# Performance work log

Measured on AMD Instinct MI355X. Metric: run time of the kernel, lower is better.

Reference implementation:

```python
import jax, jax.numpy as jnp
import numpy as np

N = 100000      # num nodes
E = 1600000     # num edges
F_IN = 602      # Reddit input features
H = 256         # num_hidden
C = 42          # num_classes


def gcn_conv(x, src, dst, W, b, num_nodes):
    """PyG GCNConv: add self loops, symmetric deg^-1/2 normalization, scatter-add."""
    h = x @ W  # [N, out] dense transform first (PyG order)
    self_idx = jnp.arange(num_nodes, dtype=src.dtype)
    s = jnp.concatenate([src, self_idx])  # [E+N]
    d = jnp.concatenate([dst, self_idx])
    deg = jax.ops.segment_sum(jnp.ones_like(d, dtype=h.dtype), d, num_segments=num_nodes)
    dinv = deg ** -0.5  # deg >= 1 due to self loops
    norm = dinv[s] * dinv[d]  # [E+N]
    msg = h[s] * norm[:, None]  # [E+N, out] gather + scale
    out = jax.ops.segment_sum(msg, d, num_segments=num_nodes)  # scatter-add
    return out + b


def setup_inputs() -> dict:
    key = jax.random.key(0)
    k = jax.random.split(key, 5)
    x = jax.random.normal(k[0], (N, F_IN), dtype=jnp.float32)
    edge_index = jax.random.randint(k[1], (2, E), 0, N, dtype=jnp.int32)
    # Glorot-style init for GCNConv linear weights; bias zeros (PyG default)
    W1 = jax.random.normal(k[2], (F_IN, H), dtype=jnp.float32) * np.float32(1.0 / np.sqrt(F_IN))
    b1 = jnp.zeros((H,), dtype=jnp.float32)
    W2 = jax.random.normal(k[3], (H, C), dtype=jnp.float32) * np.float32(1.0 / np.sqrt(H))
    b2 = jnp.zeros((C,), dtype=jnp.float32)
    return {"x": x, "edge_index": edge_index, "W1": W1, "b1": b1, "W2": W2, "b2": b2}


def reference(x, edge_index, W1, b1, W2, b2):
    src, dst = edge_index[0], edge_index[1]
    num_nodes = x.shape[0]
    h = gcn_conv(x, src, dst, W1, b1, num_nodes)
    h = jax.nn.relu(h)
    # dropout is identity in eval mode (deterministic reference)
    out = gcn_conv(h, src, dst, W2, b2, num_nodes)
    return jax.nn.log_softmax(out, axis=1)
```

## Files before the change

kernel.cpp:

```cpp
#include <hip/hip_runtime.h>
#include <stdint.h>

#define NN 100000
#define NE 1600000
#define FIN 602
#define KP1 608
#define H 256
#define C 42
#define NP2 48
#define NB1 98

typedef __bf16 bf16;
typedef __bf16 bf16x8 __attribute__((ext_vector_type(8)));
typedef float f32x4 __attribute__((ext_vector_type(4)));

__device__ __forceinline__ float b2f(bf16 v) { return (float)v; }
__device__ __forceinline__ bf16 f2b(float v) { return (bf16)v; }
__device__ __forceinline__ float us2f(unsigned short u) {
    union { unsigned int i; float f; } w; w.i = ((unsigned int)u) << 16; return w.f;
}


__global__ void k_zero(int* __restrict__ p, int n) {
    int i = blockIdx.x * 256 + threadIdx.x;
    if (i < n) p[i] = 0;
}

__global__ void k_count(const int* __restrict__ dst, int* __restrict__ cnt) {
    int e = blockIdx.x * 256 + threadIdx.x;
    if (e < NE) atomicAdd(&cnt[dst[e]], 1);
}

__global__ void k_dinv(const int* __restrict__ cnt, float* __restrict__ dinv) {
    int i = blockIdx.x * 256 + threadIdx.x;
    if (i < NN) dinv[i] = rsqrtf((float)(cnt[i] + 1));
}

__global__ __launch_bounds__(256) void k_scan1(const int* __restrict__ cnt,
                                               int* __restrict__ excl, int* __restrict__ bsum) {
    __shared__ int ts[256];
    const int tid = threadIdx.x;
    const int base = blockIdx.x * 1024 + tid * 4;
    int v[4];
#pragma unroll
    for (int j = 0; j < 4; ++j) v[j] = (base + j < NN) ? cnt[base + j] : 0;
    int s = v[0] + v[1] + v[2] + v[3];
    ts[tid] = s;
    __syncthreads();
    for (int off = 1; off < 256; off <<= 1) {
        int t = (tid >= off) ? ts[tid - off] : 0;
        __syncthreads();
        if (tid >= off) ts[tid] += t;
        __syncthreads();
    }
    int prefix = ts[tid] - s;
    if (tid == 255) bsum[blockIdx.x] = ts[255];
    int run = prefix;
#pragma unroll
    for (int j = 0; j < 4; ++j) {
        if (base + j < NN) excl[base + j] = run;
        run += v[j];
    }
}

__global__ __launch_bounds__(128) void k_scan2(int* __restrict__ bsum) {
    __shared__ int ts[128];
    const int tid = threadIdx.x;
    int v = (tid < NB1) ? bsum[tid] : 0;
    ts[tid] = v;
    __syncthreads();
    for (int off = 1; off < 128; off <<= 1) {
        int t = (tid >= off) ? ts[tid - off] : 0;
        __syncthreads();
        if (tid >= off) ts[tid] += t;
        __syncthreads();
    }
    if (tid < NB1) bsum[tid] = ts[tid] - v;
}

__global__ __launch_bounds__(256) void k_scan3(const int* __restrict__ excl, const int* __restrict__ bsum,
                                               int* __restrict__ rowptr, int* __restrict__ cursor) {
    const int tid = threadIdx.x;
    const int base = blockIdx.x * 1024 + tid * 4;
    const int add = bsum[blockIdx.x];
#pragma unroll
    for (int j = 0; j < 4; ++j) {
        int i = base + j;
        if (i < NN) { int r = excl[i] + add; rowptr[i] = r; cursor[i] = r; }
    }
    if (blockIdx.x == 0 && tid == 0) rowptr[NN] = NE;
}

__global__ void k_fill(const int* __restrict__ src, const int* __restrict__ dst,
                       int* __restrict__ cursor, int* __restrict__ esrc) {
    int e = blockIdx.x * 256 + threadIdx.x;
    if (e < NE) {
        int d = dst[e];
        int pos = atomicAdd(&cursor[d], 1);
        esrc[pos] = src[e];
    }
}


__global__ void k_transpose_w1(const float* __restrict__ w1, bf16* __restrict__ w1t) {
    int idx = blockIdx.x * 256 + threadIdx.x;
    int n = idx / KP1;
    int k = idx % KP1;
    w1t[idx] = (k < FIN) ? f2b(w1[(size_t)k * H + n]) : (bf16)0.0f;
}

__global__ void k_transpose_w2(const float* __restrict__ w2, bf16* __restrict__ w2t) {
    int idx = blockIdx.x * 256 + threadIdx.x;
    int n = idx >> 8;
    int k = idx & 255;
    w2t[idx] = (n < C) ? f2b(w2[(size_t)k * C + n]) : (bf16)0.0f;
}


__global__ __launch_bounds__(256) void k_gemm1(const float* __restrict__ x,
                                               const bf16* __restrict__ w1t,
                                               bf16* __restrict__ h1) {
    __shared__ bf16 As[64 * 32];
    const int tid = threadIdx.x;
    const int wave = tid >> 6;
    const int lane = tid & 63;
    const int q = lane >> 4;
    const int r = lane & 15;
    const int row0 = blockIdx.x * 64;

    const int srow = tid >> 2;
    const int sseg = tid & 3;
    int gsrow = row0 + srow;
    if (gsrow >= NN) gsrow = NN - 1;
    const float* xrow = x + (size_t)gsrow * FIN + sseg * 8;

    f32x4 acc[4][4];
#pragma unroll
    for (int a = 0; a < 4; ++a)
#pragma unroll
        for (int b = 0; b < 4; ++b) acc[a][b] = (f32x4){0.f, 0.f, 0.f, 0.f};

    const bf16* bbase = w1t + (size_t)(wave * 64) * KP1;

    for (int kk = 0; kk < 19; ++kk) {
        const int k0 = kk * 32;
        const int c0 = k0 + sseg * 8;
        union { bf16 s[8]; uint4 u; } pk;
        if (c0 + 8 <= FIN) {
            const float2* p = (const float2*)(xrow + k0);
            float2 f0 = p[0], f1 = p[1], f2 = p[2], f3 = p[3];
            pk.s[0] = f2b(f0.x); pk.s[1] = f2b(f0.y);
            pk.s[2] = f2b(f1.x); pk.s[3] = f2b(f1.y);
            pk.s[4] = f2b(f2.x); pk.s[5] = f2b(f2.y);
            pk.s[6] = f2b(f3.x); pk.s[7] = f2b(f3.y);
        } else {
#pragma unroll
            for (int j = 0; j < 8; ++j)
                pk.s[j] = (c0 + j < FIN) ? f2b(xrow[k0 + j]) : (bf16)0.0f;
        }
        __syncthreads();
        *(uint4*)(As + srow * 32 + sseg * 8) = pk.u;
        __syncthreads();

        bf16x8 af[4];
#pragma unroll
        for (int rt = 0; rt < 4; ++rt) {
            union { uint4 u; bf16x8 v; } ua;
            ua.u = *(const uint4*)(As + (rt * 16 + r) * 32 + q * 8);
            af[rt] = ua.v;
        }
#pragma unroll
        for (int ct = 0; ct < 4; ++ct) {
            const bf16* bp = bbase + (size_t)(ct * 16 + r) * KP1 + k0 + q * 8;
            union { uint4 u; bf16x8 v; } ub;
            ub.u = *(const uint4*)bp;
#pragma unroll
            for (int rt = 0; rt < 4; ++rt)
                acc[rt][ct] = __builtin_amdgcn_mfma_f32_16x16x32_bf16(af[rt], ub.v, acc[rt][ct], 0, 0, 0);
        }
    }

#pragma unroll
    for (int rt = 0; rt < 4; ++rt) {
#pragma unroll
        for (int ct = 0; ct < 4; ++ct) {
            const int col = wave * 64 + ct * 16 + r;
#pragma unroll
            for (int rr = 0; rr < 4; ++rr) {
                const int m = row0 + rt * 16 + q * 4 + rr;
                if (m < NN) h1[(size_t)m * H + col] = f2b(acc[rt][ct][rr]);
            }
        }
    }
}


__global__ __launch_bounds__(64) void k_gather1(const int* __restrict__ rowptr,
                                                const int* __restrict__ esrc,
                                                const bf16* __restrict__ h1,
                                                const float* __restrict__ dinv,
                                                const float* __restrict__ b1,
                                                bf16* __restrict__ hb) {
    const int n = blockIdx.x;
    const int tid = threadIdx.x;
    const float dn = dinv[n];

    uint2 u = ((const uint2*)(h1 + (size_t)n * H))[tid];
    float ws = dn * dn;
    float a0 = us2f((unsigned short)(u.x & 0xffff)) * ws;
    float a1 = us2f((unsigned short)(u.x >> 16)) * ws;
    float a2 = us2f((unsigned short)(u.y & 0xffff)) * ws;
    float a3 = us2f((unsigned short)(u.y >> 16)) * ws;

    const int beg = rowptr[n], end = rowptr[n + 1];
    int j = beg;
    for (; j + 3 < end; j += 4) {
        int s0 = esrc[j], s1 = esrc[j + 1], s2 = esrc[j + 2], s3 = esrc[j + 3];
        float w0 = dinv[s0] * dn, w1 = dinv[s1] * dn, w2 = dinv[s2] * dn, w3 = dinv[s3] * dn;
        uint2 v0 = ((const uint2*)(h1 + (size_t)s0 * H))[tid];
        uint2 v1 = ((const uint2*)(h1 + (size_t)s1 * H))[tid];
        uint2 v2 = ((const uint2*)(h1 + (size_t)s2 * H))[tid];
        uint2 v3 = ((const uint2*)(h1 + (size_t)s3 * H))[tid];
        a0 += us2f((unsigned short)(v0.x & 0xffff)) * w0;
        a1 += us2f((unsigned short)(v0.x >> 16)) * w0;
        a2 += us2f((unsigned short)(v0.y & 0xffff)) * w0;
        a3 += us2f((unsigned short)(v0.y >> 16)) * w0;
        a0 += us2f((unsigned short)(v1.x & 0xffff)) * w1;
        a1 += us2f((unsigned short)(v1.x >> 16)) * w1;
        a2 += us2f((unsigned short)(v1.y & 0xffff)) * w1;
        a3 += us2f((unsigned short)(v1.y >> 16)) * w1;
        a0 += us2f((unsigned short)(v2.x & 0xffff)) * w2;
        a1 += us2f((unsigned short)(v2.x >> 16)) * w2;
        a2 += us2f((unsigned short)(v2.y & 0xffff)) * w2;
        a3 += us2f((unsigned short)(v2.y >> 16)) * w2;
        a0 += us2f((unsigned short)(v3.x & 0xffff)) * w3;
        a1 += us2f((unsigned short)(v3.x >> 16)) * w3;
        a2 += us2f((unsigned short)(v3.y & 0xffff)) * w3;
        a3 += us2f((unsigned short)(v3.y >> 16)) * w3;
    }
    for (; j < end; ++j) {
        int s = esrc[j];
        float w = dinv[s] * dn;
        uint2 v = ((const uint2*)(h1 + (size_t)s * H))[tid];
        a0 += us2f((unsigned short)(v.x & 0xffff)) * w;
        a1 += us2f((unsigned short)(v.x >> 16)) * w;
        a2 += us2f((unsigned short)(v.y & 0xffff)) * w;
        a3 += us2f((unsigned short)(v.y >> 16)) * w;
    }

    float4 bb = ((const float4*)b1)[tid];
    a0 += bb.x; a1 += bb.y; a2 += bb.z; a3 += bb.w;
    a0 = a0 > 0.f ? a0 : 0.f;
    a1 = a1 > 0.f ? a1 : 0.f;
    a2 = a2 > 0.f ? a2 : 0.f;
    a3 = a3 > 0.f ? a3 : 0.f;

    union { unsigned short s[4]; uint2 u; } pk;
    union { bf16 b; unsigned short s; } cv;
    cv.b = f2b(a0); pk.s[0] = cv.s;
    cv.b = f2b(a1); pk.s[1] = cv.s;
    cv.b = f2b(a2); pk.s[2] = cv.s;
    cv.b = f2b(a3); pk.s[3] = cv.s;
    ((uint2*)(hb + (size_t)n * H))[tid] = pk.u;
}


__global__ __launch_bounds__(256) void k_gemm2(const bf16* __restrict__ hb,
                                               const bf16* __restrict__ w2t,
                                               bf16* __restrict__ h2) {
    __shared__ bf16 As[256 * 32];
    const int tid = threadIdx.x;
    const int wave = tid >> 6;
    const int lane = tid & 63;
    const int q = lane >> 4;
    const int r = lane & 15;
    const int row0 = blockIdx.x * 256;

    int gsrow = row0 + tid;
    if (gsrow >= NN) gsrow = NN - 1;
    const bf16* arow = hb + (size_t)gsrow * H;

    f32x4 acc[4][3];
#pragma unroll
    for (int a = 0; a < 4; ++a)
#pragma unroll
        for (int b = 0; b < 3; ++b) acc[a][b] = (f32x4){0.f, 0.f, 0.f, 0.f};

    for (int kk = 0; kk < 8; ++kk) {
        const int k0 = kk * 32;
        uint4 c0 = *(const uint4*)(arow + k0);
        uint4 c1 = *(const uint4*)(arow + k0 + 8);
        uint4 c2 = *(const uint4*)(arow + k0 + 16);
        uint4 c3 = *(const uint4*)(arow + k0 + 24);
        __syncthreads();
        uint4* ldst = (uint4*)(As + tid * 32);
        ldst[0] = c0; ldst[1] = c1; ldst[2] = c2; ldst[3] = c3;
        __syncthreads();

        bf16x8 af[4];
#pragma unroll
        for (int rt = 0; rt < 4; ++rt) {
            union { uint4 u; bf16x8 v; } ua;
            ua.u = *(const uint4*)(As + (wave * 64 + rt * 16 + r) * 32 + q * 8);
            af[rt] = ua.v;
        }
#pragma unroll
        for (int ct = 0; ct < 3; ++ct) {
            const bf16* bp = w2t + (size_t)(ct * 16 + r) * H + k0 + q * 8;
            union { uint4 u; bf16x8 v; } ub;
            ub.u = *(const uint4*)bp;
#pragma unroll
            for (int rt = 0; rt < 4; ++rt)
                acc[rt][ct] = __builtin_amdgcn_mfma_f32_16x16x32_bf16(af[rt], ub.v, acc[rt][ct], 0, 0, 0);
        }
    }

#pragma unroll
    for (int rt = 0; rt < 4; ++rt) {
#pragma unroll
        for (int ct = 0; ct < 3; ++ct) {
            const int col = ct * 16 + r;
            if (col < C) {
#pragma unroll
                for (int rr = 0; rr < 4; ++rr) {
                    const int m = row0 + wave * 64 + rt * 16 + q * 4 + rr;
                    if (m < NN) h2[(size_t)m * C + col] = f2b(acc[rt][ct][rr]);
                }
            }
        }
    }
}


__global__ __launch_bounds__(64) void k_gather2(const int* __restrict__ rowptr,
                                                const int* __restrict__ esrc,
                                                const bf16* __restrict__ h2,
                                                const float* __restrict__ dinv,
                                                const float* __restrict__ b2,
                                                float* __restrict__ out) {
    const int n = blockIdx.x;
    const int c = threadIdx.x;
    const float dn = dinv[n];

    float acc = 0.f;
    if (c < C) acc = b2f(h2[(size_t)n * C + c]) * dn * dn;

    const int beg = rowptr[n], end = rowptr[n + 1];
    int j = beg;
    for (; j + 3 < end; j += 4) {
        int s0 = esrc[j], s1 = esrc[j + 1], s2 = esrc[j + 2], s3 = esrc[j + 3];
        float w0 = dinv[s0] * dn, w1 = dinv[s1] * dn, w2 = dinv[s2] * dn, w3 = dinv[s3] * dn;
        if (c < C) {
            float v0 = b2f(h2[(size_t)s0 * C + c]);
            float v1 = b2f(h2[(size_t)s1 * C + c]);
            float v2 = b2f(h2[(size_t)s2 * C + c]);
            float v3 = b2f(h2[(size_t)s3 * C + c]);
            acc += v0 * w0 + v1 * w1 + v2 * w2 + v3 * w3;
        }
    }
    for (; j < end; ++j) {
        int s = esrc[j];
        float w = dinv[s] * dn;
        if (c < C) acc += b2f(h2[(size_t)s * C + c]) * w;
    }

    float v = (c < C) ? acc + b2[c] : -INFINITY;
    float m = v;
#pragma unroll
    for (int o = 32; o > 0; o >>= 1) m = fmaxf(m, __shfl_xor(m, o, 64));
    float ex = (c < C) ? expf(v - m) : 0.f;
    float s = ex;
#pragma unroll
    for (int o = 32; o > 0; o >>= 1) s += __shfl_xor(s, o, 64);
    if (c < C) out[(size_t)n * C + c] = (v - m) - logf(s);
}


extern "C" void kernel_launch(void* const* d_in, const int* in_sizes, int n_in,
                              void* d_out, int out_size, void* d_ws, size_t ws_size,
                              hipStream_t stream) {
    const float* x  = (const float*)d_in[0];
    const int*   ei = (const int*)d_in[1];
    const float* w1 = (const float*)d_in[2];
    const float* b1 = (const float*)d_in[3];
    const float* w2 = (const float*)d_in[4];
    const float* b2 = (const float*)d_in[5];
    float* out = (float*)d_out;

    const int* src = ei;
    const int* dst = ei + NE;

    char* base = (char*)d_ws;
    size_t off = 0;
    auto alloc = [&](size_t bytes) -> void* {
        void* p = base + off;
        off += (bytes + 255) & ~(size_t)255;
        return p;
    };
    int*   cnt    = (int*)alloc((size_t)NN * 4);
    float* dinv   = (float*)alloc((size_t)NN * 4);
    int*   excl   = (int*)alloc((size_t)NN * 4);
    int*   bsum   = (int*)alloc(128 * 4);
    int*   rowptr = (int*)alloc((size_t)(NN + 1) * 4);
    int*   cursor = (int*)alloc((size_t)NN * 4);
    int*   esrc   = (int*)alloc((size_t)NE * 4);
    bf16*  w1t    = (bf16*)alloc((size_t)H * KP1 * 2);
    bf16*  w2t    = (bf16*)alloc((size_t)NP2 * H * 2);
    bf16*  h1     = (bf16*)alloc((size_t)NN * H * 2);
    bf16*  hb     = (bf16*)alloc((size_t)NN * H * 2);
    bf16*  h2     = (bf16*)alloc((size_t)NN * C * 2);
    (void)ws_size;

    k_zero<<<dim3((NN + 255) / 256), dim3(256), 0, stream>>>(cnt, NN);
    k_count<<<dim3((NE + 255) / 256), dim3(256), 0, stream>>>(dst, cnt);
    k_dinv<<<dim3((NN + 255) / 256), dim3(256), 0, stream>>>(cnt, dinv);
    k_scan1<<<dim3(NB1), dim3(256), 0, stream>>>(cnt, excl, bsum);
    k_scan2<<<dim3(1), dim3(128), 0, stream>>>(bsum);
    k_scan3<<<dim3(NB1), dim3(256), 0, stream>>>(excl, bsum, rowptr, cursor);
    k_fill<<<dim3((NE + 255) / 256), dim3(256), 0, stream>>>(src, dst, cursor, esrc);

    k_transpose_w1<<<dim3(KP1), dim3(256), 0, stream>>>(w1, w1t);
    k_transpose_w2<<<dim3(NP2), dim3(256), 0, stream>>>(w2, w2t);

    k_gemm1<<<dim3((NN + 63) / 64), dim3(256), 0, stream>>>(x, w1t, h1);
    k_gather1<<<dim3(NN), dim3(64), 0, stream>>>(rowptr, esrc, h1, dinv, b1, hb);

    k_gemm2<<<dim3((NN + 255) / 256), dim3(256), 0, stream>>>(hb, w2t, h2);
    k_gather2<<<dim3(NN), dim3(64), 0, stream>>>(rowptr, esrc, h2, dinv, b2, out);
}
```

Before: 799.4 us.

## Prefetch GEMM A tiles into registers, pad LDS, widen gather loads

In gemm1 the K step grows to 64 with W1 padded to 640, the next x chunk is prefetched into registers while MFMAs run on the current one, and the LDS rows are padded to 72 to avoid bank conflicts. gemm2 gets the same register prefetch and LDS padding to 40. gather1 now uses 16-byte loads, with each half-wave handling alternate edges and the two halves combined by a shuffle. This is meant to hide global load latency behind compute and to halve the load instruction count in the gather, at the cost of more registers and one extra cross-lane reduction.

```diff
diff --git a/kernel.cpp b/kernel.cpp
--- a/kernel.cpp
+++ b/kernel.cpp
@@ -4,7 +4,7 @@
 #define NN 100000
 #define NE 1600000
 #define FIN 602
-#define KP1 608
+#define KP1B 640
 #define H 256
 #define C 42
 #define NP2 48
@@ -104,8 +104,8 @@
 
 __global__ void k_transpose_w1(const float* __restrict__ w1, bf16* __restrict__ w1t) {
     int idx = blockIdx.x * 256 + threadIdx.x;
-    int n = idx / KP1;
-    int k = idx % KP1;
+    int n = idx / KP1B;
+    int k = idx % KP1B;
     w1t[idx] = (k < FIN) ? f2b(w1[(size_t)k * H + n]) : (bf16)0.0f;
 }
 
@@ -120,7 +120,7 @@
 __global__ __launch_bounds__(256) void k_gemm1(const float* __restrict__ x,
                                                const bf16* __restrict__ w1t,
                                                bf16* __restrict__ h1) {
-    __shared__ bf16 As[64 * 32];
+    __shared__ bf16 As[64 * 72];
     const int tid = threadIdx.x;
     const int wave = tid >> 6;
     const int lane = tid & 63;
@@ -132,7 +132,21 @@
     const int sseg = tid & 3;
     int gsrow = row0 + srow;
     if (gsrow >= NN) gsrow = NN - 1;
-    const float* xrow = x + (size_t)gsrow * FIN + sseg * 8;
+    const float* xrow = x + (size_t)gsrow * FIN;
+
+    float pf[16];
+    auto load_chunk = [&](int kk) {
+        const int c0 = kk * 64 + sseg * 16;
+        if (c0 + 16 <= FIN) {
+            const float2* p = (const float2*)(xrow + c0);
+#pragma unroll
+            for (int jj = 0; jj < 8; ++jj) { float2 t = p[jj]; pf[2 * jj] = t.x; pf[2 * jj + 1] = t.y; }
+        } else {
+#pragma unroll
+            for (int i = 0; i < 16; ++i) pf[i] = (c0 + i < FIN) ? xrow[c0 + i] : 0.f;
+        }
+    };
+    load_chunk(0);
 
     f32x4 acc[4][4];
 #pragma unroll
@@ -140,43 +154,38 @@
 #pragma unroll
         for (int b = 0; b < 4; ++b) acc[a][b] = (f32x4){0.f, 0.f, 0.f, 0.f};
 
-    const bf16* bbase = w1t + (size_t)(wave * 64) * KP1;
-
-    for (int kk = 0; kk < 19; ++kk) {
-        const int k0 = kk * 32;
-        const int c0 = k0 + sseg * 8;
-        union { bf16 s[8]; uint4 u; } pk;
-        if (c0 + 8 <= FIN) {
-            const float2* p = (const float2*)(xrow + k0);
-            float2 f0 = p[0], f1 = p[1], f2 = p[2], f3 = p[3];
-            pk.s[0] = f2b(f0.x); pk.s[1] = f2b(f0.y);
-            pk.s[2] = f2b(f1.x); pk.s[3] = f2b(f1.y);
-            pk.s[4] = f2b(f2.x); pk.s[5] = f2b(f2.y);
-            pk.s[6] = f2b(f3.x); pk.s[7] = f2b(f3.y);
-        } else {
-#pragma unroll
-            for (int j = 0; j < 8; ++j)
-                pk.s[j] = (c0 + j < FIN) ? f2b(xrow[k0 + j]) : (bf16)0.0f;
-        }
-        __syncthreads();
-        *(uint4*)(As + srow * 32 + sseg * 8) = pk.u;
-        __syncthreads();
-
-        bf16x8 af[4];
-#pragma unroll
-        for (int rt = 0; rt < 4; ++rt) {
-            union { uint4 u; bf16x8 v; } ua;
-            ua.u = *(const uint4*)(As + (rt * 16 + r) * 32 + q * 8);
-            af[rt] = ua.v;
-        }
-#pragma unroll
-        for (int ct = 0; ct < 4; ++ct) {
-            const bf16* bp = bbase + (size_t)(ct * 16 + r) * KP1 + k0 + q * 8;
-            union { uint4 u; bf16x8 v; } ub;
-            ub.u = *(const uint4*)bp;
-#pragma unroll
-            for (int rt = 0; rt < 4; ++rt)
-                acc[rt][ct] = __builtin_amdgcn_mfma_f32_16x16x32_bf16(af[rt], ub.v, acc[rt][ct], 0, 0, 0);
+    const bf16* bbase = w1t + (size_t)(wave * 64) * KP1B;
+
+    for (int kk = 0; kk < 10; ++kk) {
+        union { bf16 s[16]; uint4 u[2]; } pk;
+#pragma unroll
+        for (int i = 0; i < 16; ++i) pk.s[i] = f2b(pf[i]);
+        __syncthreads();
+        uint4* ldst = (uint4*)(As + srow * 72 + sseg * 16);
+        ldst[0] = pk.u[0];
+        ldst[1] = pk.u[1];
+        __syncthreads();
+        if (kk < 9) load_chunk(kk + 1);
+
+#pragma unroll
+        for (int ks = 0; ks < 2; ++ks) {
+            const int kb = ks * 32 + q * 8;
+            bf16x8 af[4];
+#pragma unroll
+            for (int rt = 0; rt < 4; ++rt) {
+                union { uint4 u; bf16x8 v; } ua;
+                ua.u = *(const uint4*)(As + (rt * 16 + r) * 72 + kb);
+                af[rt] = ua.v;
+            }
+#pragma unroll
+            for (int ct = 0; ct < 4; ++ct) {
+                const bf16* bp = bbase + (size_t)(ct * 16 + r) * KP1B + kk * 64 + kb;
+                union { uint4 u; bf16x8 v; } ub;
+                ub.u = *(const uint4*)bp;
+#pragma unroll
+                for (int rt = 0; rt < 4; ++rt)
+                    acc[rt][ct] = __builtin_amdgcn_mfma_f32_16x16x32_bf16(af[rt], ub.v, acc[rt][ct], 0, 0, 0);
+            }
         }
     }
 
@@ -194,6 +203,17 @@
     }
 }
 
+
+__device__ __forceinline__ void acc8(float* a, uint4 v, float wgt) {
+    a[0] += us2f((unsigned short)(v.x & 0xffff)) * wgt;
+    a[1] += us2f((unsigned short)(v.x >> 16)) * wgt;
+    a[2] += us2f((unsigned short)(v.y & 0xffff)) * wgt;
+    a[3] += us2f((unsigned short)(v.y >> 16)) * wgt;
+    a[4] += us2f((unsigned short)(v.z & 0xffff)) * wgt;
+    a[5] += us2f((unsigned short)(v.z >> 16)) * wgt;
+    a[6] += us2f((unsigned short)(v.w & 0xffff)) * wgt;
+    a[7] += us2f((unsigned short)(v.w >> 16)) * wgt;
+}
 
 __global__ __launch_bounds__(64) void k_gather1(const int* __restrict__ rowptr,
                                                 const int* __restrict__ esrc,
@@ -202,73 +222,72 @@
                                                 const float* __restrict__ b1,
                                                 bf16* __restrict__ hb) {
     const int n = blockIdx.x;
-    const int tid = threadIdx.x;
+    const int l = threadIdx.x;
+    const int half = l >> 5;
+    const int fl = l & 31;
     const float dn = dinv[n];
 
-    uint2 u = ((const uint2*)(h1 + (size_t)n * H))[tid];
-    float ws = dn * dn;
-    float a0 = us2f((unsigned short)(u.x & 0xffff)) * ws;
-    float a1 = us2f((unsigned short)(u.x >> 16)) * ws;
-    float a2 = us2f((unsigned short)(u.y & 0xffff)) * ws;
-    float a3 = us2f((unsigned short)(u.y >> 16)) * ws;
+    float a[8];
+    {
+        uint4 u = ((const uint4*)(h1 + (size_t)n * H))[fl];
+        float ws = (half == 0) ? dn * dn : 0.f;
+        a[0] = us2f((unsigned short)(u.x & 0xffff)) * ws;
+        a[1] = us2f((unsigned short)(u.x >> 16)) * ws;
+        a[2] = us2f((unsigned short)(u.y & 0xffff)) * ws;
+        a[3] = us2f((unsigned short)(u.y >> 16)) * ws;
+        a[4] = us2f((unsigned short)(u.z & 0xffff)) * ws;
+        a[5] = us2f((unsigned short)(u.z >> 16)) * ws;
+        a[6] = us2f((unsigned short)(u.w & 0xffff)) * ws;
+        a[7] = us2f((unsigned short)(u.w >> 16)) * ws;
+    }
 
     const int beg = rowptr[n], end = rowptr[n + 1];
     int j = beg;
-    for (; j + 3 < end; j += 4) {
-        int s0 = esrc[j], s1 = esrc[j + 1], s2 = esrc[j + 2], s3 = esrc[j + 3];
+    for (; j + 8 <= end; j += 8) {
+        int s0 = esrc[j + half];
+        int s1 = esrc[j + 2 + half];
+        int s2 = esrc[j + 4 + half];
+        int s3 = esrc[j + 6 + half];
         float w0 = dinv[s0] * dn, w1 = dinv[s1] * dn, w2 = dinv[s2] * dn, w3 = dinv[s3] * dn;
-        uint2 v0 = ((const uint2*)(h1 + (size_t)s0 * H))[tid];
-        uint2 v1 = ((const uint2*)(h1 + (size_t)s1 * H))[tid];
-        uint2 v2 = ((const uint2*)(h1 + (size_t)s2 * H))[tid];
-        uint2 v3 = ((const uint2*)(h1 + (size_t)s3 * H))[tid];
-        a0 += us2f((unsigned short)(v0.x & 0xffff)) * w0;
-        a1 += us2f((unsigned short)(v0.x >> 16)) * w0;
-        a2 += us2f((unsigned short)(v0.y & 0xffff)) * w0;
-        a3 += us2f((unsigned short)(v0.y >> 16)) * w0;
-        a0 += us2f((unsigned short)(v1.x & 0xffff)) * w1;
-        a1 += us2f((unsigned short)(v1.x >> 16)) * w1;
-        a2 += us2f((unsigned short)(v1.y & 0xffff)) * w1;
-        a3 += us2f((unsigned short)(v1.y >> 16)) * w1;
-        a0 += us2f((unsigned short)(v2.x & 0xffff)) * w2;
-        a1 += us2f((unsigned short)(v2.x >> 16)) * w2;
-        a2 += us2f((unsigned short)(v2.y & 0xffff)) * w2;
-        a3 += us2f((unsigned short)(v2.y >> 16)) * w2;
-        a0 += us2f((unsigned short)(v3.x & 0xffff)) * w3;
-        a1 += us2f((unsigned short)(v3.x >> 16)) * w3;
-        a2 += us2f((unsigned short)(v3.y & 0xffff)) * w3;
-        a3 += us2f((unsigned short)(v3.y >> 16)) * w3;
-    }
-    for (; j < end; ++j) {
-        int s = esrc[j];
-        float w = dinv[s] * dn;
-        uint2 v = ((const uint2*)(h1 + (size_t)s * H))[tid];
-        a0 += us2f((unsigned short)(v.x & 0xffff)) * w;
-        a1 += us2f((unsigned short)(v.x >> 16)) * w;
-        a2 += us2f((unsigned short)(v.y & 0xffff)) * w;
-        a3 += us2f((unsigned short)(v.y >> 16)) * w;
-    }
-
-    float4 bb = ((const float4*)b1)[tid];
-    a0 += bb.x; a1 += bb.y; a2 += bb.z; a3 += bb.w;
-    a0 = a0 > 0.f ? a0 : 0.f;
-    a1 = a1 > 0.f ? a1 : 0.f;
-    a2 = a2 > 0.f ? a2 : 0.f;
-    a3 = a3 > 0.f ? a3 : 0.f;
-
-    union { unsigned short s[4]; uint2 u; } pk;
-    union { bf16 b; unsigned short s; } cv;
-    cv.b = f2b(a0); pk.s[0] = cv.s;
-    cv.b = f2b(a1); pk.s[1] = cv.s;
-    cv.b = f2b(a2); pk.s[2] = cv.s;
-    cv.b = f2b(a3); pk.s[3] = cv.s;
-    ((uint2*)(hb + (size_t)n * H))[tid] = pk.u;
+        uint4 v0 = ((const uint4*)(h1 + (size_t)s0 * H))[fl];
+        uint4 v1 = ((const uint4*)(h1 + (size_t)s1 * H))[fl];
+        uint4 v2 = ((const uint4*)(h1 + (size_t)s2 * H))[fl];
+        uint4 v3 = ((const uint4*)(h1 + (size_t)s3 * H))[fl];
+        acc8(a, v0, w0); acc8(a, v1, w1); acc8(a, v2, w2); acc8(a, v3, w3);
+    }
+    for (; j < end; j += 2) {
+        int jj = j + half;
+        if (jj < end) {
+            int s = esrc[jj];
+            float wgt = dinv[s] * dn;
+            uint4 v = ((const uint4*)(h1 + (size_t)s * H))[fl];
+            acc8(a, v, wgt);
+        }
+    }
+
+#pragma unroll
+    for (int i = 0; i < 8; ++i) a[i] += __shfl_xor(a[i], 32, 64);
+
+    if (half == 0) {
+        float4 b0 = ((const float4*)b1)[fl * 2];
+        float4 b4 = ((const float4*)b1)[fl * 2 + 1];
+        a[0] += b0.x; a[1] += b0.y; a[2] += b0.z; a[3] += b0.w;
+        a[4] += b4.x; a[5] += b4.y; a[6] += b4.z; a[7] += b4.w;
+#pragma unroll
+        for (int i = 0; i < 8; ++i) a[i] = a[i] > 0.f ? a[i] : 0.f;
+        union { unsigned short s[8]; uint4 u; } pk;
+        union { bf16 b; unsigned short s; } cv;
+#pragma unroll
+        for (int i = 0; i < 8; ++i) { cv.b = f2b(a[i]); pk.s[i] = cv.s; }
+        ((uint4*)(hb + (size_t)n * H))[fl] = pk.u;
+    }
 }
 
 
 __global__ __launch_bounds__(256) void k_gemm2(const bf16* __restrict__ hb,
                                                const bf16* __restrict__ w2t,
                                                bf16* __restrict__ h2) {
-    __shared__ bf16 As[256 * 32];
+    __shared__ bf16 As[256 * 40];
     const int tid = threadIdx.x;
     const int wave = tid >> 6;
     const int lane = tid & 63;
@@ -280,6 +299,16 @@
     if (gsrow >= NN) gsrow = NN - 1;
     const bf16* arow = hb + (size_t)gsrow * H;
 
+    uint4 c[4];
+    auto load_chunk = [&](int kk) {
+        const bf16* p = arow + kk * 32;
+        c[0] = *(const uint4*)(p);
+        c[1] = *(const uint4*)(p + 8);
+        c[2] = *(const uint4*)(p + 16);
+        c[3] = *(const uint4*)(p + 24);
+    };
+    load_chunk(0);
+
     f32x4 acc[4][3];
 #pragma unroll
     for (int a = 0; a < 4; ++a)
@@ -287,26 +316,22 @@
         for (int b = 0; b < 3; ++b) acc[a][b] = (f32x4){0.f, 0.f, 0.f, 0.f};
 
     for (int kk = 0; kk < 8; ++kk) {
-        const int k0 = kk * 32;
-        uint4 c0 = *(const uint4*)(arow + k0);
-        uint4 c1 = *(const uint4*)(arow + k0 + 8);
-        uint4 c2 = *(const uint4*)(arow + k0 + 16);
-        uint4 c3 = *(const uint4*)(arow + k0 + 24);
-        __syncthreads();
-        uint4* ldst = (uint4*)(As + tid * 32);
-        ldst[0] = c0; ldst[1] = c1; ldst[2] = c2; ldst[3] = c3;
-        __syncthreads();
+        __syncthreads();
+        uint4* ldst = (uint4*)(As + tid * 40);
+        ldst[0] = c[0]; ldst[1] = c[1]; ldst[2] = c[2]; ldst[3] = c[3];
+        __syncthreads();
+        if (kk < 7) load_chunk(kk + 1);
 
         bf16x8 af[4];
 #pragma unroll
         for (int rt = 0; rt < 4; ++rt) {
             union { uint4 u; bf16x8 v; } ua;
-            ua.u = *(const uint4*)(As + (wave * 64 + rt * 16 + r) * 32 + q * 8);
+            ua.u = *(const uint4*)(As + (wave * 64 + rt * 16 + r) * 40 + q * 8);
             af[rt] = ua.v;
         }
 #pragma unroll
         for (int ct = 0; ct < 3; ++ct) {
-            const bf16* bp = w2t + (size_t)(ct * 16 + r) * H + k0 + q * 8;
+            const bf16* bp = w2t + (size_t)(ct * 16 + r) * H + kk * 32 + q * 8;
             union { uint4 u; bf16x8 v; } ub;
             ub.u = *(const uint4*)bp;
 #pragma unroll
@@ -339,40 +364,40 @@
                                                 const float* __restrict__ b2,
                                                 float* __restrict__ out) {
     const int n = blockIdx.x;
-    const int c = threadIdx.x;
+    const int cthread = threadIdx.x;
     const float dn = dinv[n];
 
     float acc = 0.f;
-    if (c < C) acc = b2f(h2[(size_t)n * C + c]) * dn * dn;
+    if (cthread < C) acc = b2f(h2[(size_t)n * C + cthread]) * dn * dn;
 
     const int beg = rowptr[n], end = rowptr[n + 1];
     int j = beg;
     for (; j + 3 < end; j += 4) {
         int s0 = esrc[j], s1 = esrc[j + 1], s2 = esrc[j + 2], s3 = esrc[j + 3];
         float w0 = dinv[s0] * dn, w1 = dinv[s1] * dn, w2 = dinv[s2] * dn, w3 = dinv[s3] * dn;
-        if (c < C) {
-            float v0 = b2f(h2[(size_t)s0 * C + c]);
-            float v1 = b2f(h2[(size_t)s1 * C + c]);
-            float v2 = b2f(h2[(size_t)s2 * C + c]);
-            float v3 = b2f(h2[(size_t)s3 * C + c]);
+        if (cthread < C) {
+            float v0 = b2f(h2[(size_t)s0 * C + cthread]);
+            float v1 = b2f(h2[(size_t)s1 * C + cthread]);
+            float v2 = b2f(h2[(size_t)s2 * C + cthread]);
+            float v3 = b2f(h2[(size_t)s3 * C + cthread]);
             acc += v0 * w0 + v1 * w1 + v2 * w2 + v3 * w3;
         }
     }
     for (; j < end; ++j) {
         int s = esrc[j];
-        float w = dinv[s] * dn;
-        if (c < C) acc += b2f(h2[(size_t)s * C + c]) * w;
-    }
-
-    float v = (c < C) ? acc + b2[c] : -INFINITY;
+        float wgt = dinv[s] * dn;
+        if (cthread < C) acc += b2f(h2[(size_t)s * C + cthread]) * wgt;
+    }
+
+    float v = (cthread < C) ? acc + b2[cthread] : -INFINITY;
     float m = v;
 #pragma unroll
     for (int o = 32; o > 0; o >>= 1) m = fmaxf(m, __shfl_xor(m, o, 64));
-    float ex = (c < C) ? expf(v - m) : 0.f;
+    float ex = (cthread < C) ? expf(v - m) : 0.f;
     float s = ex;
 #pragma unroll
     for (int o = 32; o > 0; o >>= 1) s += __shfl_xor(s, o, 64);
-    if (c < C) out[(size_t)n * C + c] = (v - m) - logf(s);
+    if (cthread < C) out[(size_t)n * C + cthread] = (v - m) - logf(s);
 }
 
 
@@ -404,7 +429,7 @@
     int*   rowptr = (int*)alloc((size_t)(NN + 1) * 4);
     int*   cursor = (int*)alloc((size_t)NN * 4);
     int*   esrc   = (int*)alloc((size_t)NE * 4);
-    bf16*  w1t    = (bf16*)alloc((size_t)H * KP1 * 2);
+    bf16*  w1t    = (bf16*)alloc((size_t)H * KP1B * 2);
     bf16*  w2t    = (bf16*)alloc((size_t)NP2 * H * 2);
     bf16*  h1     = (bf16*)alloc((size_t)NN * H * 2);
     bf16*  hb     = (bf16*)alloc((size_t)NN * H * 2);
@@ -419,7 +444,7 @@
     k_scan3<<<dim3(NB1), dim3(256), 0, stream>>>(excl, bsum, rowptr, cursor);
     k_fill<<<dim3((NE + 255) / 256), dim3(256), 0, stream>>>(src, dst, cursor, esrc);
 
-    k_transpose_w1<<<dim3(KP1), dim3(256), 0, stream>>>(w1, w1t);
+    k_transpose_w1<<<dim3(KP1B), dim3(256), 0, stream>>>(w1, w1t);
     k_transpose_w2<<<dim3(NP2), dim3(256), 0, stream>>>(w2, w2t);
 
     k_gemm1<<<dim3((NN + 63) / 64), dim3(256), 0, stream>>>(x, w1t, h1);
```

Result: slower. 833.5 us (+4.3%).
